# Kernel optimization log

Measured on AMD Instinct MI355X. Metric: run time of the kernel, lower is better.

Reference implementation:

```python
import jax, jax.numpy as jnp
import numpy as np

N_NODES = 100000
N_EDGES = 1000000
F_IN = 256
HEADS = 2
C_OUT = 64
NEG_SLOPE = 0.2


def setup_inputs() -> dict:
    key = jax.random.key(0)
    k_x, k_e, k_ws, k_wd, k_a = jax.random.split(key, 5)
    x = jax.random.normal(k_x, (N_NODES, F_IN), dtype=jnp.float32)
    edge_index = jax.random.randint(k_e, (2, N_EDGES), 0, N_NODES, dtype=jnp.int64)
    # uniform init as in init_randoms('uniform'), scale is irrelevant for correctness
    W_src = jax.random.uniform(k_ws, (F_IN, HEADS * C_OUT), dtype=jnp.float32, minval=-0.1, maxval=0.1)
    W_dst = jax.random.uniform(k_wd, (F_IN, HEADS * C_OUT), dtype=jnp.float32, minval=-0.1, maxval=0.1)
    att = jax.random.uniform(k_a, (HEADS, C_OUT), dtype=jnp.float32, minval=-0.1, maxval=0.1)
    bias = jnp.zeros((HEADS * C_OUT,), dtype=jnp.float32)
    return {"x": x, "edge_index": edge_index, "W_src": W_src, "W_dst": W_dst, "att": att, "bias": bias}


def reference(x, edge_index, W_src, W_dst, att, bias):
    # GATv2 conv (MyGATConv), concat=True, add_self_loops=False, dropout=0
    N = x.shape[0]
    H, C = att.shape
    x_src = (x @ W_src).reshape(N, H, C)  # Theta_s x  [N,H,C]
    x_dst = (x @ W_dst).reshape(N, H, C)  # Theta_d x  [N,H,C]
    src = edge_index[0]  # j (source)
    dst = edge_index[1]  # i (target) -> segment index

    xj = x_src[src]                                   # [E,H,C]
    e = jax.nn.leaky_relu(xj + x_dst[dst], NEG_SLOPE)  # [E,H,C]
    logits = jnp.einsum('ehc,hc->eh', e, att)          # [E,H]

    # segment softmax over destination neighborhoods
    seg_max = jax.ops.segment_max(logits, dst, num_segments=N)  # [N,H]
    seg_max = jnp.where(jnp.isfinite(seg_max), seg_max, 0.0)
    ex = jnp.exp(logits - seg_max[dst])                # [E,H]
    denom = jax.ops.segment_sum(ex, dst, num_segments=N)  # [N,H]
    alpha = ex / (denom[dst] + 1e-16)                  # [E,H]

    # scatter-add aggregation of alpha * Theta_s x_j
    out = jax.ops.segment_sum(alpha[:, :, None] * xj, dst, num_segments=N)  # [N,H,C]
    return out.reshape(N, H * C) + bias
```

## Files before the change

### kernel.cpp

```cpp
#include <hip/hip_runtime.h>

#define F_IN 256
#define HC   128

typedef __attribute__((ext_vector_type(8))) short bf16x8;
typedef __attribute__((ext_vector_type(4))) float f32x4;

__device__ __forceinline__ unsigned short f2b(float f) {
    unsigned int u = __float_as_uint(f);
    return (unsigned short)((u + 0x7FFFu + ((u >> 16) & 1u)) >> 16);
}

__device__ __forceinline__ unsigned int f2b_pk(float lo, float hi) {
    unsigned int ul = __float_as_uint(lo);
    unsigned int uh = __float_as_uint(hi);
    ul = ul + 0x7FFFu + ((ul >> 16) & 1u);
    uh = uh + 0x7FFFu + ((uh >> 16) & 1u);
    return __builtin_amdgcn_perm(uh, ul, 0x07060302);
}

#define DPP_ADD(x, ctrl) \
    x += __int_as_float(__builtin_amdgcn_update_dpp(0, __float_as_int(x), ctrl, 0xF, 0xF, true))

__device__ __forceinline__ float row_sum16(float x) {
    DPP_ADD(x, 0xB1);
    DPP_ADD(x, 0x4E);
    DPP_ADD(x, 0x141);
    DPP_ADD(x, 0x140);
    return x;
}

__global__ __launch_bounds__(256) void k_prep(const float* __restrict__ Ws,
                                              const float* __restrict__ Wd,
                                              unsigned short* __restrict__ PB) {
    int tid = blockIdx.x * 256 + threadIdx.x;
    int nt  = tid >> 9;
    int rem = tid & 511;
    int t   = rem >> 6;
    int l   = rem & 63;
    int m   = l & 15;
    int w   = nt >> 2;
    int g   = nt & 3;
    int pos = w * 64 + m * 4 + g;
    int kbase = 32 * t + (l >> 4) * 8;

    const float* W;
    int n;
    if (pos < 128) {
        W = Ws; n = (pos & 1) * 64 + (pos >> 1);
    } else {
        int p2 = pos - 128;
        W = Wd; n = (p2 & 1) * 64 + (p2 >> 1);
    }
    union { bf16x8 v; unsigned short u[8]; } o;
#pragma unroll
    for (int j = 0; j < 8; ++j)
        o.u[j] = f2b(W[(kbase + j) * HC + n]);
    *(bf16x8*)(PB + (size_t)tid * 8) = o.v;
}

#define LIST_BLOCKS 2048
__global__ __launch_bounds__(256) void k_gemm_list(const float* __restrict__ x,
                                                   const unsigned short* __restrict__ PB,
                                                   unsigned short* __restrict__ xsrc_pk,
                                                   unsigned short* __restrict__ xdst_pk, int N,
                                                   const int* __restrict__ src,
                                                   const int* __restrict__ dst, int E,
                                                   int* __restrict__ head4,
                                                   uint2* __restrict__ rec) {
    if (blockIdx.x < LIST_BLOCKS) {
        int i = blockIdx.x * 256 + threadIdx.x;
        int stride = LIST_BLOCKS * 256;
        for (; i < E; i += stride) {
            int d = dst[i];
            int s = src[i];
            int old = atomicExch(&head4[(size_t)d * 4 + (i & 3)], i);
            rec[i] = make_uint2((unsigned int)old, (unsigned int)s);
        }
        return;
    }

    const int wave = threadIdx.x >> 6;
    const int lane = threadIdx.x & 63;
    const int m = lane & 15;
    const int q = lane >> 4;
    const long row0 = (long)(blockIdx.x - LIST_BLOCKS) * 32;

    f32x4 acc[2][4];
#pragma unroll
    for (int a = 0; a < 2; ++a)
#pragma unroll
        for (int b = 0; b < 4; ++b) acc[a][b] = (f32x4){0.f, 0.f, 0.f, 0.f};

    long rl[2];
#pragma unroll
    for (int mt = 0; mt < 2; ++mt) {
        long r = row0 + mt * 16 + m;
        rl[mt] = (r < N) ? r : (long)(N - 1);
    }

#pragma unroll
    for (int t = 0; t < 8; ++t) {
        const int k0 = t * 32 + q * 8;
        bf16x8 af[2];
#pragma unroll
        for (int mt = 0; mt < 2; ++mt) {
            const float* p = x + rl[mt] * F_IN + k0;
            float4 a = *(const float4*)p;
            float4 c = *(const float4*)(p + 4);
            union { bf16x8 v; unsigned int u[4]; } cv;
            cv.u[0] = f2b_pk(a.x, a.y);
            cv.u[1] = f2b_pk(a.z, a.w);
            cv.u[2] = f2b_pk(c.x, c.y);
            cv.u[3] = f2b_pk(c.z, c.w);
            af[mt] = cv.v;
        }
#pragma unroll
        for (int g = 0; g < 4; ++g) {
            const int nt = wave * 4 + g;
            bf16x8 bf = *(const bf16x8*)(PB + ((size_t)(nt * 8 + t) * 64 + lane) * 8);
            acc[0][g] = __builtin_amdgcn_mfma_f32_16x16x32_bf16(af[0], bf, acc[0][g], 0, 0, 0);
            acc[1][g] = __builtin_amdgcn_mfma_f32_16x16x32_bf16(af[1], bf, acc[1][g], 0, 0, 0);
        }
    }

    unsigned short* dstArr = (wave < 2) ? xsrc_pk : xdst_pk;
    const int colOff = ((wave & 1) * 64) + m * 4;
#pragma unroll
    for (int mt = 0; mt < 2; ++mt) {
#pragma unroll
        for (int r = 0; r < 4; ++r) {
            long row = row0 + mt * 16 + q * 4 + r;
            if (row >= N) continue;
            uint2 v;
            v.x = f2b_pk(acc[mt][0][r], acc[mt][1][r]);
            v.y = f2b_pk(acc[mt][2][r], acc[mt][3][r]);
            *(uint2*)(dstArr + row * HC + colOff) = v;
        }
    }
}

__global__ __launch_bounds__(256) void k_agg(const unsigned int* __restrict__ xsrc_u,
                                             const unsigned int* __restrict__ xdst_u,
                                             const int* __restrict__ head4,
                                             const uint2* __restrict__ rec,
                                             const float* __restrict__ att,
                                             const float* __restrict__ bias,
                                             float* __restrict__ out, int N) {
    int wid  = threadIdx.x >> 6;
    int lane = threadIdx.x & 63;
    int node = blockIdx.x * 4 + wid;
    if (node >= N) return;
    int g = lane >> 4;
    int s = lane & 15;

    uint4 D = *(const uint4*)(xdst_u + (size_t)node * 64 + s * 4);
    float xd0[4], xd1[4];
    {
        unsigned int du[4] = {D.x, D.y, D.z, D.w};
#pragma unroll
        for (int k = 0; k < 4; ++k) {
            xd0[k] = __uint_as_float(du[k] << 16);
            xd1[k] = __uint_as_float(du[k] & 0xFFFF0000u);
        }
    }
    float4 A0 = *(const float4*)(att + s * 4);
    float4 A1 = *(const float4*)(att + 64 + s * 4);
    float c10[4] = {0.6f * A0.x, 0.6f * A0.y, 0.6f * A0.z, 0.6f * A0.w};
    float c20[4] = {0.4f * A0.x, 0.4f * A0.y, 0.4f * A0.z, 0.4f * A0.w};
    float c11[4] = {0.6f * A1.x, 0.6f * A1.y, 0.6f * A1.z, 0.6f * A1.w};
    float c21[4] = {0.4f * A1.x, 0.4f * A1.y, 0.4f * A1.z, 0.4f * A1.w};

    float l0 = 0.f, l1 = 0.f;
    float o0[4] = {0.f, 0.f, 0.f, 0.f}, o1[4] = {0.f, 0.f, 0.f, 0.f};

    int e = head4[(size_t)node * 4 + g];
    uint2 r;
    if (e >= 0) r = rec[e];
    while (__any(e >= 0)) {
        if (e >= 0) {
            int j = (int)r.y;
            uint4 U = *(const uint4*)(xsrc_u + (size_t)j * 64 + s * 4);
            int en = (int)r.x;
            if (en >= 0) r = rec[en];
            unsigned int cu[4] = {U.x, U.y, U.z, U.w};
            float xj0[4], xj1[4];
            float s0 = 0.f, s1 = 0.f;
#pragma unroll
            for (int k = 0; k < 4; ++k) {
                xj0[k] = __uint_as_float(cu[k] << 16);
                xj1[k] = __uint_as_float(cu[k] & 0xFFFF0000u);
                float e0 = xj0[k] + xd0[k];
                float e1 = xj1[k] + xd1[k];
                s0 = fmaf(c10[k], e0, s0); s0 = fmaf(c20[k], fabsf(e0), s0);
                s1 = fmaf(c11[k], e1, s1); s1 = fmaf(c21[k], fabsf(e1), s1);
            }
            s0 = row_sum16(s0);
            s1 = row_sum16(s1);
            float w0 = __expf(s0);
            float w1 = __expf(s1);
            l0 += w0; l1 += w1;
#pragma unroll
            for (int k = 0; k < 4; ++k) {
                o0[k] = fmaf(w0, xj0[k], o0[k]);
                o1[k] = fmaf(w1, xj1[k], o1[k]);
            }
            e = en;
        }
    }

#define XRED(v) { v += __shfl_xor(v, 16, 64); v += __shfl_xor(v, 32, 64); }
    XRED(l0); XRED(l1);
#pragma unroll
    for (int k = 0; k < 4; ++k) { XRED(o0[k]); XRED(o1[k]); }
#undef XRED

    if (g == 0) {
        float inv0 = __builtin_amdgcn_rcpf(l0 + 1e-16f);
        float inv1 = __builtin_amdgcn_rcpf(l1 + 1e-16f);
        float4 B0 = *(const float4*)(bias + s * 4);
        float4 B1 = *(const float4*)(bias + 64 + s * 4);
        float4 R0 = {o0[0] * inv0 + B0.x, o0[1] * inv0 + B0.y,
                     o0[2] * inv0 + B0.z, o0[3] * inv0 + B0.w};
        float4 R1 = {o1[0] * inv1 + B1.x, o1[1] * inv1 + B1.y,
                     o1[2] * inv1 + B1.z, o1[3] * inv1 + B1.w};
        *(float4*)(out + (size_t)node * HC + s * 4) = R0;
        *(float4*)(out + (size_t)node * HC + 64 + s * 4) = R1;
    }
}

extern "C" void kernel_launch(void* const* d_in, const int* in_sizes, int n_in,
                              void* d_out, int out_size, void* d_ws, size_t ws_size,
                              hipStream_t stream) {
    const float* x    = (const float*)d_in[0];
    const int*   ei   = (const int*)d_in[1];
    const float* Ws   = (const float*)d_in[2];
    const float* Wd   = (const float*)d_in[3];
    const float* att  = (const float*)d_in[4];
    const float* bias = (const float*)d_in[5];
    float* out = (float*)d_out;

    const int N = in_sizes[0] / F_IN;
    const int E = in_sizes[1] / 2;
    const int* src = ei;
    const int* dst = ei + E;

    char* ws = (char*)d_ws;
    size_t off = 0;
    auto alloc = [&](size_t bytes) -> char* {
        off = (off + 255) & ~(size_t)255;
        char* p = ws + off;
        off += bytes;
        return p;
    };
    unsigned short* xsrc_pk = (unsigned short*)alloc((size_t)N * HC * sizeof(unsigned short));
    unsigned short* xdst_pk = (unsigned short*)alloc((size_t)N * HC * sizeof(unsigned short));
    unsigned short* PB = (unsigned short*)alloc(256 * 256 * sizeof(unsigned short));
    int*   head4 = (int*)alloc((size_t)N * 4 * sizeof(int));
    uint2* rec   = (uint2*)alloc((size_t)E * sizeof(uint2));

    hipMemsetAsync(head4, 0xFF, (size_t)N * 4 * sizeof(int), stream);

    k_prep<<<32, 256, 0, stream>>>(Ws, Wd, PB);
    k_gemm_list<<<LIST_BLOCKS + (N + 31) / 32, 256, 0, stream>>>(
        x, PB, xsrc_pk, xdst_pk, N, src, dst, E, head4, rec);
    k_agg<<<(N + 3) / 4, 256, 0, stream>>>((const unsigned int*)xsrc_pk,
                                           (const unsigned int*)xdst_pk,
                                           head4, rec, att, bias, out, N);
}
```

Before: 323.0 us.

## Stage bf16 x tiles in swizzled LDS and double GEMM rows per block

The GEMM part now loads a 64-row tile of x once with coalesced float4 reads, converts it to bf16 and stores it in XOR-swizzled shared memory. Each wave then reads A fragments from LDS and issues four M-tiles per B fragment, so every PB load feeds twice as many MFMAs. Before, each wave fetched x straight from global memory with strided per-lane reads. The list-building block count is also halved. The cost is 32KB of LDS per block and a barrier, which may lower occupancy.

New measurement: 290.5 us. -10.0%, faster.

```diff
diff --git a/kernel.cpp b/kernel.cpp
--- a/kernel.cpp
+++ b/kernel.cpp
@@ -59,7 +59,7 @@
     *(bf16x8*)(PB + (size_t)tid * 8) = o.v;
 }
 
-#define LIST_BLOCKS 2048
+#define LIST_BLOCKS 1024
 __global__ __launch_bounds__(256) void k_gemm_list(const float* __restrict__ x,
                                                    const unsigned short* __restrict__ PB,
                                                    unsigned short* __restrict__ xsrc_pk,
@@ -80,54 +80,61 @@
         return;
     }
 
+    __shared__ unsigned short smem[64 * F_IN];
+    char* sb = (char*)smem;
+
     const int wave = threadIdx.x >> 6;
     const int lane = threadIdx.x & 63;
     const int m = lane & 15;
     const int q = lane >> 4;
-    const long row0 = (long)(blockIdx.x - LIST_BLOCKS) * 32;
-
-    f32x4 acc[2][4];
-#pragma unroll
-    for (int a = 0; a < 2; ++a)
+    const long row0 = (long)(blockIdx.x - LIST_BLOCKS) * 64;
+
+    {
+        const int col = lane * 4;
+        const int wbyte_base = col * 2;
+#pragma unroll 8
+        for (int i = 0; i < 16; ++i) {
+            int row = i * 4 + wave;
+            long grow = row0 + row;
+            if (grow >= N) grow = N - 1;
+            float4 a = *(const float4*)(x + grow * F_IN + col);
+            uint2 v;
+            v.x = f2b_pk(a.x, a.y);
+            v.y = f2b_pk(a.z, a.w);
+            *(uint2*)(sb + row * 512 + (wbyte_base ^ ((row & 7) << 4))) = v;
+        }
+    }
+    __syncthreads();
+
+    f32x4 acc[4][4];
+#pragma unroll
+    for (int a = 0; a < 4; ++a)
 #pragma unroll
         for (int b = 0; b < 4; ++b) acc[a][b] = (f32x4){0.f, 0.f, 0.f, 0.f};
 
-    long rl[2];
-#pragma unroll
-    for (int mt = 0; mt < 2; ++mt) {
-        long r = row0 + mt * 16 + m;
-        rl[mt] = (r < N) ? r : (long)(N - 1);
-    }
-
 #pragma unroll
     for (int t = 0; t < 8; ++t) {
-        const int k0 = t * 32 + q * 8;
-        bf16x8 af[2];
-#pragma unroll
-        for (int mt = 0; mt < 2; ++mt) {
-            const float* p = x + rl[mt] * F_IN + k0;
-            float4 a = *(const float4*)p;
-            float4 c = *(const float4*)(p + 4);
-            union { bf16x8 v; unsigned int u[4]; } cv;
-            cv.u[0] = f2b_pk(a.x, a.y);
-            cv.u[1] = f2b_pk(a.z, a.w);
-            cv.u[2] = f2b_pk(c.x, c.y);
-            cv.u[3] = f2b_pk(c.z, c.w);
-            af[mt] = cv.v;
+        const int bytein = t * 64 + q * 16;
+        bf16x8 af[4];
+#pragma unroll
+        for (int mt = 0; mt < 4; ++mt) {
+            const int row = mt * 16 + m;
+            af[mt] = *(const bf16x8*)(sb + row * 512 + (bytein ^ ((row & 7) << 4)));
         }
 #pragma unroll
         for (int g = 0; g < 4; ++g) {
             const int nt = wave * 4 + g;
             bf16x8 bf = *(const bf16x8*)(PB + ((size_t)(nt * 8 + t) * 64 + lane) * 8);
-            acc[0][g] = __builtin_amdgcn_mfma_f32_16x16x32_bf16(af[0], bf, acc[0][g], 0, 0, 0);
-            acc[1][g] = __builtin_amdgcn_mfma_f32_16x16x32_bf16(af[1], bf, acc[1][g], 0, 0, 0);
+#pragma unroll
+            for (int mt = 0; mt < 4; ++mt)
+                acc[mt][g] = __builtin_amdgcn_mfma_f32_16x16x32_bf16(af[mt], bf, acc[mt][g], 0, 0, 0);
         }
     }
 
     unsigned short* dstArr = (wave < 2) ? xsrc_pk : xdst_pk;
     const int colOff = ((wave & 1) * 64) + m * 4;
 #pragma unroll
-    for (int mt = 0; mt < 2; ++mt) {
+    for (int mt = 0; mt < 4; ++mt) {
 #pragma unroll
         for (int r = 0; r < 4; ++r) {
             long row = row0 + mt * 16 + q * 4 + r;
@@ -262,7 +269,7 @@
     hipMemsetAsync(head4, 0xFF, (size_t)N * 4 * sizeof(int), stream);
 
     k_prep<<<32, 256, 0, stream>>>(Ws, Wd, PB);
-    k_gemm_list<<<LIST_BLOCKS + (N + 31) / 32, 256, 0, stream>>>(
+    k_gemm_list<<<LIST_BLOCKS + (int)((N + 63) / 64), 256, 0, stream>>>(
         x, PB, xsrc_pk, xdst_pk, N, src, dst, E, head4, rec);
     k_agg<<<(N + 3) / 4, 256, 0, stream>>>((const unsigned int*)xsrc_pk,
                                            (const unsigned int*)xdst_pk,
```
